# Optimization experiments

Measured on AMD Instinct MI355X. Metric: run time of the kernel, lower is better.

## Reference

```python
import jax, jax.numpy as jnp
import numpy as np

N, L, E, H = 4, 1024, 1024, 32
HD = E // H  # head_dim == heads by construction (32)


def setup_inputs() -> dict:
    key = jax.random.key(0)
    ks = jax.random.split(key, 8)
    values = jax.random.normal(ks[0], (N, L, E), dtype=jnp.float32)
    keys = jax.random.normal(ks[1], (N, L, E), dtype=jnp.float32)
    query = jax.random.normal(ks[2], (N, L, E), dtype=jnp.float32)
    mask = jnp.ones((N, 1, 1, L), dtype=jnp.int32)
    # per-head projection weights (torch Linear, no bias): y = x @ W.T
    s = 1.0 / np.sqrt(HD)
    Wv = jax.random.uniform(ks[3], (HD, HD), jnp.float32, -s, s)
    Wk = jax.random.uniform(ks[4], (HD, HD), jnp.float32, -s, s)
    Wq = jax.random.uniform(ks[5], (HD, HD), jnp.float32, -s, s)
    se = 1.0 / np.sqrt(E)
    Wo = jax.random.uniform(ks[6], (E, E), jnp.float32, -se, se)
    bo = jax.random.uniform(ks[7], (E,), jnp.float32, -se, se)
    return {"values": values, "keys": keys, "query": query, "mask": mask,
            "Wv": Wv, "Wk": Wk, "Wq": Wq, "Wo": Wo, "bo": bo}


def reference(values, keys, query, mask, Wv, Wk, Wq, Wo, bo):
    n = query.shape[0]
    # reshape (N, L, H, HD) then per-head linear projections (x @ W.T)
    v = values.reshape(n, -1, H, HD) @ Wv.T
    k = keys.reshape(n, -1, H, HD) @ Wk.T
    q = query.reshape(n, -1, H, HD) @ Wq.T
    # full score matrix [N, H, Q, K]
    energy = jnp.einsum('nqhd,nkhd->nhqk', q, k)
    energy = jnp.where(mask == 0, jnp.float32(-1e20), energy)
    attention = jax.nn.softmax(energy / jnp.sqrt(jnp.float32(E)), axis=3)
    out = jnp.einsum('nhql,nlhd->nqhd', attention, v)
    out = out.reshape(n, -1, H * HD)
    return out @ Wo.T + bo
```

## Files before the change

kernel.cpp:

```cpp
#include <hip/hip_runtime.h>
#include <hip/hip_bf16.h>

#define N_ 4
#define L_ 1024
#define E_ 1024
#define H_ 32
#define HD_ 32

typedef unsigned short ushort;
typedef __attribute__((ext_vector_type(8))) short short8;
typedef __attribute__((ext_vector_type(4))) float float4v;
typedef __attribute__((ext_vector_type(2))) unsigned int uint2v;
typedef __attribute__((ext_vector_type(2))) float float2v;

__device__ __forceinline__ unsigned packbf2(float a, float b) {
    unsigned ua = __float_as_uint(a);
    unsigned ub = __float_as_uint(b);
    ua += 0x7FFFu + ((ua >> 16) & 1u);
    ub += 0x7FFFu + ((ub >> 16) & 1u);
    return (ua >> 16) | (ub & 0xFFFF0000u);
}

__device__ __forceinline__ ushort f2b(float f) {
    unsigned u = __float_as_uint(f);
    u += 0x7FFFu + ((u >> 16) & 1u);
    return (ushort)(u >> 16);
}

__device__ __forceinline__ float fast_exp2(float x) {
#if __has_builtin(__builtin_amdgcn_exp2f)
    return __builtin_amdgcn_exp2f(x);
#else
    return __expf(x * 0.69314718056f);
#endif
}

__device__ __forceinline__ short8 cvt8(const float* __restrict__ p) {
    float4v a = *(const float4v*)p;
    float4v b = *(const float4v*)(p + 4);
    union { unsigned u[4]; short8 s; } r;
    r.u[0] = packbf2(a[0], a[1]); r.u[1] = packbf2(a[2], a[3]);
    r.u[2] = packbf2(b[0], b[1]); r.u[3] = packbf2(b[2], b[3]);
    return r.s;
}

__global__ __launch_bounds__(256) void proj_kernel(
    const float* __restrict__ v_in, const float* __restrict__ k_in,
    const float* __restrict__ q_in,
    const float* __restrict__ Wv, const float* __restrict__ Wk,
    const float* __restrict__ Wq, const float* __restrict__ Wo,
    const int* __restrict__ mask,
    ushort* __restrict__ vt_ws, ushort* __restrict__ k_ws,
    ushort* __restrict__ q_ws, ushort* __restrict__ wo_bf,
    float* __restrict__ bias_f)
{
    const int n = blockIdx.z, h = blockIdx.y, l0 = blockIdx.x * 64;
    const int t = threadIdx.x, wave = t >> 6, lane = t & 63;
    const int m = lane & 15, g = lane >> 4;

    {
        const int lb = ((n * H_ + h) << 4) + blockIdx.x;
        const int i = lb * 256 + t;
        float2v w2 = *(const float2v*)(Wo + 2 * i);
        ((unsigned*)wo_bf)[i] = packbf2(w2[0], w2[1]);
    }
    if (h == 0 && t < 64)
        bias_f[n * L_ + l0 + t] = (mask[n * L_ + l0 + t] == 0) ? -1e30f : 0.0f;

    const size_t row = (size_t)(n * L_) + l0 + wave * 16 + m;
    const float* src[3] = {v_in, k_in, q_in};
    const float* wsrc[3] = {Wv, Wk, Wq};

    short8 Xf[3], Wf[3][2];
#pragma unroll
    for (int mat = 0; mat < 3; ++mat) {
        Xf[mat] = cvt8(src[mat] + row * E_ + h * HD_ + g * 8);
#pragma unroll
        for (int dt = 0; dt < 2; ++dt)
            Wf[mat][dt] = cvt8(wsrc[mat] + (dt * 16 + m) * HD_ + g * 8);
    }

    const size_t obase = (size_t)(n * H_ + h) * L_;
    const size_t vb = (size_t)(n * H_ + h) * HD_ * L_;
    const int tok = l0 + wave * 16 + m;

#pragma unroll
    for (int mat = 1; mat < 3; ++mat) {
        ushort* outp = (mat == 1) ? k_ws : q_ws;
#pragma unroll
        for (int dt = 0; dt < 2; ++dt) {
            float4v z = float4v{0.f, 0.f, 0.f, 0.f};
            float4v acc = __builtin_amdgcn_mfma_f32_16x16x32_bf16(Wf[mat][dt], Xf[mat], z, 0, 0, 0);
            uint2v pk;
            pk[0] = packbf2(acc[0], acc[1]);
            pk[1] = packbf2(acc[2], acc[3]);
            *(uint2v*)(outp + (obase + tok) * HD_ + dt * 16 + g * 4) = pk;
        }
    }
#pragma unroll
    for (int dt = 0; dt < 2; ++dt) {
        float4v z = float4v{0.f, 0.f, 0.f, 0.f};
        float4v acc = __builtin_amdgcn_mfma_f32_16x16x32_bf16(Wf[0][dt], Xf[0], z, 0, 0, 0);
#pragma unroll
        for (int r = 0; r < 4; ++r) {
            int d = dt * 16 + g * 4 + r;
            vt_ws[vb + (size_t)d * L_ + tok] = f2b(acc[r]);
        }
    }
}

__global__ __launch_bounds__(256, 4) void attn_kernel(
    const ushort* __restrict__ q_ws, const ushort* __restrict__ k_ws,
    const ushort* __restrict__ vt_ws, const float* __restrict__ bias_f,
    ushort* __restrict__ x_ws)
{
    const int B = blockIdx.x;
    const int head = ((B >> 6) << 3) + (B & 7);
    const int qt = (B >> 3) & 7;
    const int n = head >> 5, h = head & 31, q0 = qt * 128;

    const int t = threadIdx.x, wave = t >> 6, lane = t & 63;
    const int m = lane & 15, g = lane >> 4;

    __shared__ ushort sP[4][2][2][16][72];

    const size_t base = (size_t)(n * H_ + h) * L_;
    const ushort* vb_p = vt_ws + (size_t)(n * H_ + h) * HD_ * L_;

    short8 qfa = *(const short8*)(q_ws + (base + q0 + wave * 16 + m) * HD_ + g * 8);
    short8 qfb = *(const short8*)(q_ws + (base + q0 + 64 + wave * 16 + m) * HD_ + g * 8);

    float4v Oa[2], Ob[2];
    Oa[0] = float4v{0.f,0.f,0.f,0.f}; Oa[1] = float4v{0.f,0.f,0.f,0.f};
    Ob[0] = float4v{0.f,0.f,0.f,0.f}; Ob[1] = float4v{0.f,0.f,0.f,0.f};
    float rsa[4] = {0.f,0.f,0.f,0.f}, rsb[4] = {0.f,0.f,0.f,0.f};
    const float k1 = 0.03125f * 1.44269504f;

    ushort* const pa0 = &sP[wave][0][0][m][0];
    ushort* const pa1 = &sP[wave][1][0][m][0];
    ushort* const pb0 = &sP[wave][0][1][m][0];
    ushort* const pb1 = &sP[wave][1][1][m][0];

    const ushort* kp = k_ws + base * HD_ + (size_t)m * HD_ + g * 8;
    const ushort* vp = vb_p + (size_t)m * L_ + g * 8;
    const float*  bp = bias_f + n * L_ + g * 4;

    short8 kf[4];
#pragma unroll
    for (int nb = 0; nb < 4; ++nb)
        kf[nb] = *(const short8*)(kp + (size_t)nb * 16 * HD_);
    kp += (size_t)64 * HD_;

    float4v b4[4];
#pragma unroll
    for (int nb = 0; nb < 4; ++nb)
        b4[nb] = *(const float4v*)(bp + nb * 16);
    bp += 64;

    float4v Sa[4], Sb[4];
#pragma unroll
    for (int nb = 0; nb < 4; ++nb) {
        float4v z = float4v{0.f,0.f,0.f,0.f};
        Sa[nb] = __builtin_amdgcn_mfma_f32_16x16x32_bf16(kf[nb], qfa, z, 0, 0, 0);
        Sb[nb] = __builtin_amdgcn_mfma_f32_16x16x32_bf16(kf[nb], qfb, z, 0, 0, 0);
    }
#pragma unroll
    for (int nb = 0; nb < 4; ++nb)
        kf[nb] = *(const short8*)(kp + (size_t)nb * 16 * HD_);
    kp += (size_t)64 * HD_;
    short8 vf[2][2];
#pragma unroll
    for (int kb = 0; kb < 2; ++kb)
#pragma unroll
        for (int db = 0; db < 2; ++db)
            vf[kb][db] = *(const short8*)(vp + (size_t)db * 16 * L_ + kb * 32);
    vp += 64;
    __builtin_amdgcn_sched_barrier(0);

#pragma unroll
    for (int nb = 0; nb < 4; ++nb) {
        float a0 = fast_exp2(fmaf(Sa[nb][0], k1, b4[nb][0]));
        float a1 = fast_exp2(fmaf(Sa[nb][1], k1, b4[nb][1]));
        float a2 = fast_exp2(fmaf(Sa[nb][2], k1, b4[nb][2]));
        float a3 = fast_exp2(fmaf(Sa[nb][3], k1, b4[nb][3]));
        rsa[0] += a0; rsa[1] += a1; rsa[2] += a2; rsa[3] += a3;
        uint2v pk; pk[0] = packbf2(a0, a1); pk[1] = packbf2(a2, a3);
        *(uint2v*)(pa0 + nb * 16 + g * 4) = pk;
        float e0 = fast_exp2(fmaf(Sb[nb][0], k1, b4[nb][0]));
        float e1 = fast_exp2(fmaf(Sb[nb][1], k1, b4[nb][1]));
        float e2 = fast_exp2(fmaf(Sb[nb][2], k1, b4[nb][2]));
        float e3 = fast_exp2(fmaf(Sb[nb][3], k1, b4[nb][3]));
        rsb[0] += e0; rsb[1] += e1; rsb[2] += e2; rsb[3] += e3;
        uint2v qk; qk[0] = packbf2(e0, e1); qk[1] = packbf2(e2, e3);
        *(uint2v*)(pb0 + nb * 16 + g * 4) = qk;
    }

    for (int c = 1; c < 16; ++c) {
#pragma unroll
        for (int nb = 0; nb < 4; ++nb)
            b4[nb] = *(const float4v*)(bp + nb * 16);
        bp += 64;

#pragma unroll
        for (int nb = 0; nb < 4; ++nb) {
            float4v z = float4v{0.f,0.f,0.f,0.f};
            Sa[nb] = __builtin_amdgcn_mfma_f32_16x16x32_bf16(kf[nb], qfa, z, 0, 0, 0);
        }

        const ushort* ra = (c & 1) ? pa0 : pa1;
#pragma unroll
        for (int kb = 0; kb < 2; ++kb) {
            short8 af = *(const short8*)(ra + kb * 32 + g * 8);
            Oa[0] = __builtin_amdgcn_mfma_f32_16x16x32_bf16(af, vf[kb][0], Oa[0], 0, 0, 0);
            Oa[1] = __builtin_amdgcn_mfma_f32_16x16x32_bf16(af, vf[kb][1], Oa[1], 0, 0, 0);
        }

        ushort* wa = (c & 1) ? pa1 : pa0;
#pragma unroll
        for (int nb = 0; nb < 4; ++nb) {
            float a0 = fast_exp2(fmaf(Sa[nb][0], k1, b4[nb][0]));
            float a1 = fast_exp2(fmaf(Sa[nb][1], k1, b4[nb][1]));
            float a2 = fast_exp2(fmaf(Sa[nb][2], k1, b4[nb][2]));
            float a3 = fast_exp2(fmaf(Sa[nb][3], k1, b4[nb][3]));
            rsa[0] += a0; rsa[1] += a1; rsa[2] += a2; rsa[3] += a3;
            uint2v pk; pk[0] = packbf2(a0, a1); pk[1] = packbf2(a2, a3);
            *(uint2v*)(wa + nb * 16 + g * 4) = pk;
        }

#pragma unroll
        for (int nb = 0; nb < 4; ++nb) {
            float4v z = float4v{0.f,0.f,0.f,0.f};
            Sb[nb] = __builtin_amdgcn_mfma_f32_16x16x32_bf16(kf[nb], qfb, z, 0, 0, 0);
        }
#pragma unroll
        for (int nb = 0; nb < 4; ++nb)
            kf[nb] = *(const short8*)(kp + (size_t)nb * 16 * HD_);
        kp += (size_t)64 * HD_;

        const ushort* rb = (c & 1) ? pb0 : pb1;
#pragma unroll
        for (int kb = 0; kb < 2; ++kb) {
            short8 bf = *(const short8*)(rb + kb * 32 + g * 8);
            Ob[0] = __builtin_amdgcn_mfma_f32_16x16x32_bf16(bf, vf[kb][0], Ob[0], 0, 0, 0);
            Ob[1] = __builtin_amdgcn_mfma_f32_16x16x32_bf16(bf, vf[kb][1], Ob[1], 0, 0, 0);
        }
#pragma unroll
        for (int kb = 0; kb < 2; ++kb)
#pragma unroll
            for (int db = 0; db < 2; ++db)
                vf[kb][db] = *(const short8*)(vp + (size_t)db * 16 * L_ + kb * 32);
        vp += 64;

        __builtin_amdgcn_sched_barrier(0);

        ushort* wb = (c & 1) ? pb1 : pb0;
#pragma unroll
        for (int nb = 0; nb < 4; ++nb) {
            float e0 = fast_exp2(fmaf(Sb[nb][0], k1, b4[nb][0]));
            float e1 = fast_exp2(fmaf(Sb[nb][1], k1, b4[nb][1]));
            float e2 = fast_exp2(fmaf(Sb[nb][2], k1, b4[nb][2]));
            float e3 = fast_exp2(fmaf(Sb[nb][3], k1, b4[nb][3]));
            rsb[0] += e0; rsb[1] += e1; rsb[2] += e2; rsb[3] += e3;
            uint2v qk; qk[0] = packbf2(e0, e1); qk[1] = packbf2(e2, e3);
            *(uint2v*)(wb + nb * 16 + g * 4) = qk;
        }
    }

#pragma unroll
    for (int kb = 0; kb < 2; ++kb) {
        short8 af = *(const short8*)(pa1 + kb * 32 + g * 8);
        Oa[0] = __builtin_amdgcn_mfma_f32_16x16x32_bf16(af, vf[kb][0], Oa[0], 0, 0, 0);
        Oa[1] = __builtin_amdgcn_mfma_f32_16x16x32_bf16(af, vf[kb][1], Oa[1], 0, 0, 0);
    }
#pragma unroll
    for (int kb = 0; kb < 2; ++kb) {
        short8 bf = *(const short8*)(pb1 + kb * 32 + g * 8);
        Ob[0] = __builtin_amdgcn_mfma_f32_16x16x32_bf16(bf, vf[kb][0], Ob[0], 0, 0, 0);
        Ob[1] = __builtin_amdgcn_mfma_f32_16x16x32_bf16(bf, vf[kb][1], Ob[1], 0, 0, 0);
    }

    float ra = (rsa[0] + rsa[1]) + (rsa[2] + rsa[3]);
    float rb = (rsb[0] + rsb[1]) + (rsb[2] + rsb[3]);
    ra += __shfl_xor(ra, 16, 64); ra += __shfl_xor(ra, 32, 64);
    rb += __shfl_xor(rb, 16, 64); rb += __shfl_xor(rb, 32, 64);
#pragma unroll
    for (int r = 0; r < 4; ++r) {
        float inva = 1.f / __shfl(ra, g * 4 + r, 64);
        float invb = 1.f / __shfl(rb, g * 4 + r, 64);
        size_t rowa = (size_t)n * L_ + q0 + wave * 16 + g * 4 + r;
        size_t rowb = rowa + 64;
#pragma unroll
        for (int db = 0; db < 2; ++db) {
            x_ws[rowa * E_ + h * HD_ + db * 16 + m] = f2b(Oa[db][r] * inva);
            x_ws[rowb * E_ + h * HD_ + db * 16 + m] = f2b(Ob[db][r] * invb);
        }
    }
}

__global__ __launch_bounds__(256) void out_gemm_kernel(
    const ushort* __restrict__ X, const ushort* __restrict__ wo_bf,
    const float* __restrict__ bo, float* __restrict__ C)
{
    const int B = blockIdx.x;
    const int it = ((B >> 7) << 3) + (B & 7);
    const int jt = (B >> 3) & 15;
    const int i0 = it * 64, j0 = jt * 64;

    const int t = threadIdx.x, wave = t >> 6, lane = t & 63;
    const int m = lane & 15, g = lane >> 4;

    __shared__ ushort sA[64][72];
    __shared__ ushort sB[64][72];

    float4v acc[4];
#pragma unroll
    for (int nb = 0; nb < 4; ++nb) acc[nb] = float4v{0.f,0.f,0.f,0.f};

    const int r0 = t >> 2;
    const int c0 = (t & 3) * 16;

    const ushort* xp = X + (size_t)(i0 + r0) * E_ + c0;
    const ushort* wp = wo_bf + (size_t)(j0 + r0) * E_ + c0;

    short8 xr0 = *(const short8*)xp;
    short8 xr1 = *(const short8*)(xp + 8);
    short8 wr0 = *(const short8*)wp;
    short8 wr1 = *(const short8*)(wp + 8);

    for (int k0 = 0; k0 < E_; k0 += 64) {
        __syncthreads();
        *(short8*)&sA[r0][c0]     = xr0;
        *(short8*)&sA[r0][c0 + 8] = xr1;
        *(short8*)&sB[r0][c0]     = wr0;
        *(short8*)&sB[r0][c0 + 8] = wr1;
        __syncthreads();
        if (k0 + 64 < E_) {
            xr0 = *(const short8*)(xp + k0 + 64);
            xr1 = *(const short8*)(xp + k0 + 72);
            wr0 = *(const short8*)(wp + k0 + 64);
            wr1 = *(const short8*)(wp + k0 + 72);
        }
#pragma unroll
        for (int kb = 0; kb < 2; ++kb) {
            short8 afr = *(const short8*)&sA[wave * 16 + m][kb * 32 + g * 8];
#pragma unroll
            for (int nb = 0; nb < 4; ++nb) {
                short8 bfr = *(const short8*)&sB[nb * 16 + m][kb * 32 + g * 8];
                acc[nb] = __builtin_amdgcn_mfma_f32_16x16x32_bf16(afr, bfr, acc[nb], 0, 0, 0);
            }
        }
    }

#pragma unroll
    for (int nb = 0; nb < 4; ++nb) {
        int col = j0 + nb * 16 + m;
        float bias = bo[col];
#pragma unroll
        for (int r = 0; r < 4; ++r) {
            int rowi = i0 + wave * 16 + g * 4 + r;
            C[(size_t)rowi * E_ + col] = acc[nb][r] + bias;
        }
    }
}

extern "C" void kernel_launch(void* const* d_in, const int* in_sizes, int n_in,
                              void* d_out, int out_size, void* d_ws, size_t ws_size,
                              hipStream_t stream) {
    const float* values = (const float*)d_in[0];
    const float* keys   = (const float*)d_in[1];
    const float* query  = (const float*)d_in[2];
    const int*   mask   = (const int*)d_in[3];
    const float* Wv     = (const float*)d_in[4];
    const float* Wk     = (const float*)d_in[5];
    const float* Wq     = (const float*)d_in[6];
    const float* Wo     = (const float*)d_in[7];
    const float* bo     = (const float*)d_in[8];
    float* out = (float*)d_out;

    const size_t M4 = (size_t)N_ * H_ * L_ * HD_;
    ushort* q_ws   = (ushort*)d_ws;
    ushort* k_ws   = q_ws + M4;
    ushort* vt_ws  = k_ws + M4;
    ushort* x_ws   = vt_ws + M4;
    ushort* wo_bf  = x_ws + M4;
    float*  bias_f = (float*)(wo_bf + (size_t)E_ * E_);

    proj_kernel<<<dim3(L_ / 64, H_, N_), 256, 0, stream>>>(
        values, keys, query, Wv, Wk, Wq, Wo, mask,
        vt_ws, k_ws, q_ws, wo_bf, bias_f);

    attn_kernel<<<dim3(1024), 256, 0, stream>>>(
        q_ws, k_ws, vt_ws, bias_f, x_ws);

    out_gemm_kernel<<<dim3(1024), 256, 0, stream>>>(
        x_ws, wo_bf, bo, out);
}
```

Baseline: 213.3 us.

## Stage K/V tiles through LDS with async global_load_lds double buffering

The attention kernel now cooperatively loads each 64-key K tile and V^T tile into shared memory using direct global-to-LDS loads, double-buffered two tiles ahead, instead of every wave loading its own K/V fragments from global memory. The mask bias row is also staged into LDS once per block. The V tile uses an XOR swizzle to avoid bank conflicts, and the software pipeline is restructured so the P tile is written and consumed within the same iteration. This is meant to remove the redundant per-wave global loads of K/V, at the cost of two block barriers per iteration and the loss of the previous cross-iteration overlap between exp and MFMA.

```diff
diff --git a/kernel.cpp b/kernel.cpp
--- a/kernel.cpp
+++ b/kernel.cpp
@@ -42,6 +42,12 @@
     r.u[0] = packbf2(a[0], a[1]); r.u[1] = packbf2(a[2], a[3]);
     r.u[2] = packbf2(b[0], b[1]); r.u[3] = packbf2(b[2], b[3]);
     return r.s;
+}
+
+typedef __attribute__((address_space(1))) const unsigned int as1_u32;
+typedef __attribute__((address_space(3))) unsigned int as3_u32;
+__device__ __forceinline__ void g2l16(const void* gp, void* lp) {
+    __builtin_amdgcn_global_load_lds((as1_u32*)gp, (as3_u32*)lp, 16, 0, 0);
 }
 
 __global__ __launch_bounds__(256) void proj_kernel(
@@ -122,13 +128,31 @@
     const int t = threadIdx.x, wave = t >> 6, lane = t & 63;
     const int m = lane & 15, g = lane >> 4;
 
-    __shared__ ushort sP[4][2][2][16][72];
+    __shared__ ushort sK[2][64][32];
+    __shared__ ushort sV[2][32][64];
+    __shared__ ushort sP[4][2][16][72];
+    __shared__ float  sB4[L_];
 
     const size_t base = (size_t)(n * H_ + h) * L_;
-    const ushort* vb_p = vt_ws + (size_t)(n * H_ + h) * HD_ * L_;
+    const ushort* vtb = vt_ws + (size_t)(n * H_ + h) * HD_ * L_;
 
     short8 qfa = *(const short8*)(q_ws + (base + q0 + wave * 16 + m) * HD_ + g * 8);
     short8 qfb = *(const short8*)(q_ws + (base + q0 + 64 + wave * 16 + m) * HD_ + g * 8);
+    {
+        float4v b = *(const float4v*)(bias_f + n * L_ + t * 4);
+        *(float4v*)&sB4[t * 4] = b;
+    }
+
+    const ushort* kgp = k_ws + base * HD_ + (size_t)t * 8;
+    const ushort* vgp = vtb + (size_t)(t >> 3) * L_
+                            + (((t & 7) ^ ((t >> 3) & 7)) << 3);
+
+    g2l16(kgp,             &sK[0][wave * 16][0]);
+    g2l16(vgp,             &sV[0][wave * 8][0]);
+    g2l16(kgp + 64 * HD_,  &sK[1][wave * 16][0]);
+    g2l16(vgp + 64,        &sV[1][wave * 8][0]);
+
+    asm volatile("s_waitcnt lgkmcnt(0)" ::: "memory");
 
     float4v Oa[2], Ob[2];
     Oa[0] = float4v{0.f,0.f,0.f,0.f}; Oa[1] = float4v{0.f,0.f,0.f,0.f};
@@ -136,86 +160,43 @@
     float rsa[4] = {0.f,0.f,0.f,0.f}, rsb[4] = {0.f,0.f,0.f,0.f};
     const float k1 = 0.03125f * 1.44269504f;
 
-    ushort* const pa0 = &sP[wave][0][0][m][0];
-    ushort* const pa1 = &sP[wave][1][0][m][0];
-    ushort* const pb0 = &sP[wave][0][1][m][0];
-    ushort* const pb1 = &sP[wave][1][1][m][0];
-
-    const ushort* kp = k_ws + base * HD_ + (size_t)m * HD_ + g * 8;
-    const ushort* vp = vb_p + (size_t)m * L_ + g * 8;
-    const float*  bp = bias_f + n * L_ + g * 4;
-
-    short8 kf[4];
-#pragma unroll
-    for (int nb = 0; nb < 4; ++nb)
-        kf[nb] = *(const short8*)(kp + (size_t)nb * 16 * HD_);
-    kp += (size_t)64 * HD_;
-
-    float4v b4[4];
-#pragma unroll
-    for (int nb = 0; nb < 4; ++nb)
-        b4[nb] = *(const float4v*)(bp + nb * 16);
-    bp += 64;
-
-    float4v Sa[4], Sb[4];
-#pragma unroll
-    for (int nb = 0; nb < 4; ++nb) {
-        float4v z = float4v{0.f,0.f,0.f,0.f};
-        Sa[nb] = __builtin_amdgcn_mfma_f32_16x16x32_bf16(kf[nb], qfa, z, 0, 0, 0);
-        Sb[nb] = __builtin_amdgcn_mfma_f32_16x16x32_bf16(kf[nb], qfb, z, 0, 0, 0);
-    }
-#pragma unroll
-    for (int nb = 0; nb < 4; ++nb)
-        kf[nb] = *(const short8*)(kp + (size_t)nb * 16 * HD_);
-    kp += (size_t)64 * HD_;
-    short8 vf[2][2];
-#pragma unroll
-    for (int kb = 0; kb < 2; ++kb)
-#pragma unroll
-        for (int db = 0; db < 2; ++db)
-            vf[kb][db] = *(const short8*)(vp + (size_t)db * 16 * L_ + kb * 32);
-    vp += 64;
-    __builtin_amdgcn_sched_barrier(0);
-
-#pragma unroll
-    for (int nb = 0; nb < 4; ++nb) {
-        float a0 = fast_exp2(fmaf(Sa[nb][0], k1, b4[nb][0]));
-        float a1 = fast_exp2(fmaf(Sa[nb][1], k1, b4[nb][1]));
-        float a2 = fast_exp2(fmaf(Sa[nb][2], k1, b4[nb][2]));
-        float a3 = fast_exp2(fmaf(Sa[nb][3], k1, b4[nb][3]));
-        rsa[0] += a0; rsa[1] += a1; rsa[2] += a2; rsa[3] += a3;
-        uint2v pk; pk[0] = packbf2(a0, a1); pk[1] = packbf2(a2, a3);
-        *(uint2v*)(pa0 + nb * 16 + g * 4) = pk;
-        float e0 = fast_exp2(fmaf(Sb[nb][0], k1, b4[nb][0]));
-        float e1 = fast_exp2(fmaf(Sb[nb][1], k1, b4[nb][1]));
-        float e2 = fast_exp2(fmaf(Sb[nb][2], k1, b4[nb][2]));
-        float e3 = fast_exp2(fmaf(Sb[nb][3], k1, b4[nb][3]));
-        rsb[0] += e0; rsb[1] += e1; rsb[2] += e2; rsb[3] += e3;
-        uint2v qk; qk[0] = packbf2(e0, e1); qk[1] = packbf2(e2, e3);
-        *(uint2v*)(pb0 + nb * 16 + g * 4) = qk;
-    }
-
-    for (int c = 1; c < 16; ++c) {
+    ushort* const pa = &sP[wave][0][m][0];
+    ushort* const pb = &sP[wave][1][m][0];
+    const int xsw = (m & 7) << 3;
+
+    for (int c = 0; c < 16; ++c) {
+        const int buf = c & 1;
+
+        if (c < 15) asm volatile("s_waitcnt vmcnt(2)" ::: "memory");
+        else        asm volatile("s_waitcnt vmcnt(0)" ::: "memory");
+        __builtin_amdgcn_s_barrier();
+
+        short8 kf[4];
 #pragma unroll
         for (int nb = 0; nb < 4; ++nb)
-            b4[nb] = *(const float4v*)(bp + nb * 16);
-        bp += 64;
-
+            kf[nb] = *(const short8*)&sK[buf][nb * 16 + m][g * 8];
+
+        float4v Sa[4], Sb[4];
 #pragma unroll
         for (int nb = 0; nb < 4; ++nb) {
             float4v z = float4v{0.f,0.f,0.f,0.f};
             Sa[nb] = __builtin_amdgcn_mfma_f32_16x16x32_bf16(kf[nb], qfa, z, 0, 0, 0);
-        }
-
-        const ushort* ra = (c & 1) ? pa0 : pa1;
-#pragma unroll
-        for (int kb = 0; kb < 2; ++kb) {
-            short8 af = *(const short8*)(ra + kb * 32 + g * 8);
-            Oa[0] = __builtin_amdgcn_mfma_f32_16x16x32_bf16(af, vf[kb][0], Oa[0], 0, 0, 0);
-            Oa[1] = __builtin_amdgcn_mfma_f32_16x16x32_bf16(af, vf[kb][1], Oa[1], 0, 0, 0);
-        }
-
-        ushort* wa = (c & 1) ? pa1 : pa0;
+            Sb[nb] = __builtin_amdgcn_mfma_f32_16x16x32_bf16(kf[nb], qfb, z, 0, 0, 0);
+        }
+
+        float4v b4[4];
+#pragma unroll
+        for (int nb = 0; nb < 4; ++nb)
+            b4[nb] = *(const float4v*)&sB4[c * 64 + nb * 16 + g * 4];
+
+        short8 vf[2][2];
+#pragma unroll
+        for (int kb = 0; kb < 2; ++kb)
+#pragma unroll
+            for (int db = 0; db < 2; ++db)
+                vf[kb][db] = *(const short8*)
+                    &sV[buf][db * 16 + m][(kb * 32 + g * 8) ^ xsw];
+
 #pragma unroll
         for (int nb = 0; nb < 4; ++nb) {
             float a0 = fast_exp2(fmaf(Sa[nb][0], k1, b4[nb][0]));
@@ -224,36 +205,15 @@
             float a3 = fast_exp2(fmaf(Sa[nb][3], k1, b4[nb][3]));
             rsa[0] += a0; rsa[1] += a1; rsa[2] += a2; rsa[3] += a3;
             uint2v pk; pk[0] = packbf2(a0, a1); pk[1] = packbf2(a2, a3);
-            *(uint2v*)(wa + nb * 16 + g * 4) = pk;
-        }
-
-#pragma unroll
-        for (int nb = 0; nb < 4; ++nb) {
-            float4v z = float4v{0.f,0.f,0.f,0.f};
-            Sb[nb] = __builtin_amdgcn_mfma_f32_16x16x32_bf16(kf[nb], qfb, z, 0, 0, 0);
-        }
-#pragma unroll
-        for (int nb = 0; nb < 4; ++nb)
-            kf[nb] = *(const short8*)(kp + (size_t)nb * 16 * HD_);
-        kp += (size_t)64 * HD_;
-
-        const ushort* rb = (c & 1) ? pb0 : pb1;
+            *(uint2v*)(pa + nb * 16 + g * 4) = pk;
+        }
 #pragma unroll
         for (int kb = 0; kb < 2; ++kb) {
-            short8 bf = *(const short8*)(rb + kb * 32 + g * 8);
-            Ob[0] = __builtin_amdgcn_mfma_f32_16x16x32_bf16(bf, vf[kb][0], Ob[0], 0, 0, 0);
-            Ob[1] = __builtin_amdgcn_mfma_f32_16x16x32_bf16(bf, vf[kb][1], Ob[1], 0, 0, 0);
-        }
-#pragma unroll
-        for (int kb = 0; kb < 2; ++kb)
-#pragma unroll
-            for (int db = 0; db < 2; ++db)
-                vf[kb][db] = *(const short8*)(vp + (size_t)db * 16 * L_ + kb * 32);
-        vp += 64;
-
-        __builtin_amdgcn_sched_barrier(0);
-
-        ushort* wb = (c & 1) ? pb1 : pb0;
+            short8 af = *(const short8*)(pa + kb * 32 + g * 8);
+            Oa[0] = __builtin_amdgcn_mfma_f32_16x16x32_bf16(af, vf[kb][0], Oa[0], 0, 0, 0);
+            Oa[1] = __builtin_amdgcn_mfma_f32_16x16x32_bf16(af, vf[kb][1], Oa[1], 0, 0, 0);
+        }
+
 #pragma unroll
         for (int nb = 0; nb < 4; ++nb) {
             float e0 = fast_exp2(fmaf(Sb[nb][0], k1, b4[nb][0]));
@@ -261,22 +221,22 @@
             float e2 = fast_exp2(fmaf(Sb[nb][2], k1, b4[nb][2]));
             float e3 = fast_exp2(fmaf(Sb[nb][3], k1, b4[nb][3]));
             rsb[0] += e0; rsb[1] += e1; rsb[2] += e2; rsb[3] += e3;
-            uint2v qk; qk[0] = packbf2(e0, e1); qk[1] = packbf2(e2, e3);
-            *(uint2v*)(wb + nb * 16 + g * 4) = qk;
-        }
-    }
-
-#pragma unroll
-    for (int kb = 0; kb < 2; ++kb) {
-        short8 af = *(const short8*)(pa1 + kb * 32 + g * 8);
-        Oa[0] = __builtin_amdgcn_mfma_f32_16x16x32_bf16(af, vf[kb][0], Oa[0], 0, 0, 0);
-        Oa[1] = __builtin_amdgcn_mfma_f32_16x16x32_bf16(af, vf[kb][1], Oa[1], 0, 0, 0);
-    }
-#pragma unroll
-    for (int kb = 0; kb < 2; ++kb) {
-        short8 bf = *(const short8*)(pb1 + kb * 32 + g * 8);
-        Ob[0] = __builtin_amdgcn_mfma_f32_16x16x32_bf16(bf, vf[kb][0], Ob[0], 0, 0, 0);
-        Ob[1] = __builtin_amdgcn_mfma_f32_16x16x32_bf16(bf, vf[kb][1], Ob[1], 0, 0, 0);
+            uint2v pk; pk[0] = packbf2(e0, e1); pk[1] = packbf2(e2, e3);
+            *(uint2v*)(pb + nb * 16 + g * 4) = pk;
+        }
+#pragma unroll
+        for (int kb = 0; kb < 2; ++kb) {
+            short8 bf = *(const short8*)(pb + kb * 32 + g * 8);
+            Ob[0] = __builtin_amdgcn_mfma_f32_16x16x32_bf16(bf, vf[kb][0], Ob[0], 0, 0, 0);
+            Ob[1] = __builtin_amdgcn_mfma_f32_16x16x32_bf16(bf, vf[kb][1], Ob[1], 0, 0, 0);
+        }
+
+        if (c < 14) {
+            __builtin_amdgcn_s_barrier();
+            __builtin_amdgcn_sched_barrier(0);
+            g2l16(kgp + (size_t)(c + 2) * 64 * HD_, &sK[buf][wave * 16][0]);
+            g2l16(vgp + (c + 2) * 64,               &sV[buf][wave * 8][0]);
+        }
     }
 
     float ra = (rsa[0] + rsa[1]) + (rsa[2] + rsa[3]);
```

Result: faster. 178.3 us (-16.4%).
